# Performance work log

Measured on AMD Instinct MI355X. Metric: run time of the kernel, lower is better.

## Reference

```python
import jax, jax.numpy as jnp
import numpy as np

ALPHA = 0.5  # learn_alpha=False -> constant

def _init(key, shape, fan_in):
    return jax.random.normal(key, shape, dtype=jnp.float32) / np.sqrt(fan_in)

def setup_inputs() -> dict:
    key = jax.random.key(0)
    ks = jax.random.split(key, 12)
    B, S, N, F, H, E = 4, 8, 4000, 64, 128, 32000
    x_seq = jax.random.normal(ks[0], (B, S, N, F), dtype=jnp.float32)
    edge_index = jax.random.randint(ks[1], (B, S, 2, E), 0, N, dtype=jnp.int32)
    edge_weight = jax.random.uniform(ks[2], (B, S, E), dtype=jnp.float32)
    params = dict(
        W0_s=_init(ks[3], (H, F), F), b0_s=jnp.zeros((H,), jnp.float32),
        W0_d=_init(ks[4], (H, F), F), b0_d=jnp.zeros((H,), jnp.float32),
        W1_s=_init(ks[5], (H, H), H), b1_s=jnp.zeros((H,), jnp.float32),
        W1_d=_init(ks[6], (H, H), H), b1_d=jnp.zeros((H,), jnp.float32),
        lstm_Wih=_init(ks[7], (4 * H, H), H), lstm_Whh=_init(ks[8], (4 * H, H), H),
        lstm_bih=jnp.zeros((4 * H,), jnp.float32), lstm_bhh=jnp.zeros((4 * H,), jnp.float32),
        Wp=_init(ks[9], (F, H), H), bp=jnp.zeros((F,), jnp.float32),
    )
    return {"x_seq": x_seq, "edge_index": edge_index, "edge_weight": edge_weight, **params}

def _dir_gcn(x, src, dst, ew, Ws, bs, Wd, bd):
    # x: [N, Fin]. DirGCN: alpha * W_s(A_hat x) + (1-alpha) * W_d(A_hat^T x)
    # with symmetric directed normalization D_out^{-1/2} A D_in^{-1/2}.
    N = x.shape[0]
    deg_out = jax.ops.segment_sum(ew, src, num_segments=N)
    deg_in = jax.ops.segment_sum(ew, dst, num_segments=N)
    inv_out = jnp.where(deg_out > 0, jax.lax.rsqrt(jnp.maximum(deg_out, 1e-12)), 0.0)
    inv_in = jnp.where(deg_in > 0, jax.lax.rsqrt(jnp.maximum(deg_in, 1e-12)), 0.0)
    norm = ew * inv_out[src] * inv_in[dst]                         # [E]
    agg_f = jax.ops.segment_sum(norm[:, None] * x[src], dst, num_segments=N)  # A_hat x
    agg_b = jax.ops.segment_sum(norm[:, None] * x[dst], src, num_segments=N)  # A_hat^T x
    return ALPHA * (agg_f @ Ws.T + bs) + (1.0 - ALPHA) * (agg_b @ Wd.T + bd)

def reference(x_seq, edge_index, edge_weight, W0_s, b0_s, W0_d, b0_d,
              W1_s, b1_s, W1_d, b1_d, lstm_Wih, lstm_Whh, lstm_bih, lstm_bhh, Wp, bp):
    B, S, N, F = x_seq.shape
    H = W0_s.shape[0]
    G = B * S
    # fuse the per-(batch, timestep) python loops into one batched graph pass
    x = x_seq.reshape(G, N, F)
    src = edge_index[:, :, 0, :].reshape(G, -1)
    dst = edge_index[:, :, 1, :].reshape(G, -1)
    ew = edge_weight.reshape(G, -1)
    conv = jax.vmap(_dir_gcn, in_axes=(0, 0, 0, 0, None, None, None, None))
    h = conv(x, src, dst, ew, W0_s, b0_s, W0_d, b0_d)   # dropout is a no-op in eval mode
    h = conv(h, src, dst, ew, W1_s, b1_s, W1_d, b1_d)   # [G, N, H]
    # faithful to original: [B, S*N, H].reshape(B*N, S, H) (order-preserving flatten)
    seq = h.reshape(B * N, S, H)
    # single-layer unidirectional LSTM, batch_first; pytorch gate order i,f,g,o
    def step(carry, x_t):
        hprev, c = carry
        gates = x_t @ lstm_Wih.T + lstm_bih + hprev @ lstm_Whh.T + lstm_bhh
        i, f, g, o = jnp.split(gates, 4, axis=-1)
        c = jax.nn.sigmoid(f) * c + jax.nn.sigmoid(i) * jnp.tanh(g)
        hn = jax.nn.sigmoid(o) * jnp.tanh(c)
        return (hn, c), None
    h0 = jnp.zeros((B * N, H), x_seq.dtype)
    (h_last, _), _ = jax.lax.scan(step, (h0, h0), seq.transpose(1, 0, 2))
    return h_last.reshape(B, N, H) @ Wp.T + bp           # [B, N, num_features]
```

## Files before the change

### kernel.cpp

```cpp
#include <hip/hip_runtime.h>
#include <hip/hip_bf16.h>

#define B_  4
#define S_  8
#define N_  4000
#define F_  64
#define H_  128
#define E_  32000
#define G_  (B_*S_)
#define GN_ (G_*N_)
#define M_  (B_*N_)
#define GE_ (G_*E_)
#define HALF_GN 64000
#define HALF_M  8000
#define NBLK_   8
#define EPB_    (E_/NBLK_)

#define OFF_W0S 0
#define OFF_B0S 8192
#define OFF_W0D 8320
#define OFF_B0D 16512
#define OFF_W1S 16640
#define OFF_B1S 33024
#define OFF_W1D 33152
#define OFF_B1D 49536
#define OFF_WIH 49664
#define OFF_WHH 115200
#define OFF_BIH 180736
#define OFF_BHH 181248
#define OFF_WP  181760
#define OFF_BP  189952
#define WCV_TOTAL 190016

#define WS_FLAG   0
#define WS_WCV    16
#define WS_WPH    190032
#define WS_WPC    222800
#define WS_BIASC  288336
#define WS_DEGO   288848
#define WS_DEGI   416848
#define WS_CNTI   544848
#define WS_CNTO   672848
#define WS_RPI    800848
#define WS_RPO    928880
#define WS_CSRI   1312912
#define WS_CSRO   3360912
#define WS_X2     5408912
#define WS_PART   9608912
#define WS_HB     21792912
#define WS_GT     29984912
#define WS_WC0    46368912

typedef __attribute__((ext_vector_type(8))) short bf16x8;
typedef __attribute__((ext_vector_type(4))) float f32x4;
typedef __attribute__((ext_vector_type(8))) unsigned short ushort8;

__device__ inline float bfu2f(unsigned short u){ union{unsigned int i; float f;} v; v.i=((unsigned int)u)<<16; return v.f; }
__device__ inline unsigned short f2bfu(float f){ __hip_bfloat16 b = __float2bfloat16(f); return *(unsigned short*)&b; }
__device__ inline float rcpf(float x){ return __builtin_amdgcn_rcpf(x); }
__device__ inline float sigmf(float x){ return rcpf(1.0f + __expf(-x)); }
__device__ inline float tanhfast(float x){ return 1.0f - 2.0f*rcpf(1.0f + __expf(2.0f*x)); }
__device__ inline float loadf(const void* p, long i, int isf32){
    return isf32 ? ((const float*)p)[i]
                 : __bfloat162float(((const __hip_bfloat16*)p)[i]);
}
__device__ inline float4 cvtbf4(ushort4 u){
    float4 f;
    f.x = __uint_as_float(((unsigned)u.x)<<16);
    f.y = __uint_as_float(((unsigned)u.y)<<16);
    f.z = __uint_as_float(((unsigned)u.z)<<16);
    f.w = __uint_as_float(((unsigned)u.w)<<16);
    return f;
}

__global__ void sniff_kernel(const unsigned int* __restrict__ ew, int* __restrict__ flag){
    __shared__ int s;
    if (threadIdx.x == 0) s = 0;
    __syncthreads();
    unsigned int lo = ew[threadIdx.x] & 0xFFFFu;
    if (lo > 0x3F80u) atomicOr(&s, 1);
    __syncthreads();
    if (threadIdx.x == 0) flag[0] = s;
}

struct WSeg { const void* src; int base; int n; };
struct WDesc { WSeg seg[14]; };
__global__ void convert_weights(WDesc d, float* __restrict__ dst, const int* __restrict__ flag){
    int isf32 = flag[0];
    int idx = blockIdx.x*256 + threadIdx.x;
    #pragma unroll
    for (int s=0;s<14;s++){
        int off = idx - d.seg[s].base;
        if (off >= 0 && off < d.seg[s].n){
            dst[idx] = loadf(d.seg[s].src, off, isf32);
            return;
        }
    }
}

__global__ void repack_whh(const float* __restrict__ wcv, unsigned short* __restrict__ whb){
    int idx = blockIdx.x*256 + threadIdx.x;
    whb[idx] = f2bfu(wcv[OFF_WHH + idx]);
}

__global__ void repack_wc0(const float* __restrict__ wcv, unsigned short* __restrict__ wc0){
    int idx = blockIdx.x*256 + threadIdx.x;
    int k = idx & 127, n = idx >> 7;
    float v = (k < 64) ? 0.5f*wcv[OFF_W0S + n*64 + k] : 0.5f*wcv[OFF_W0D + n*64 + (k-64)];
    wc0[idx] = f2bfu(v);
}

__global__ void xcvt_kernel(const void* __restrict__ x, const int* __restrict__ flag,
                            unsigned short* __restrict__ Xb){
    long idx = (long)blockIdx.x*256 + threadIdx.x;
    if (idx >= (long)GN_*64) return;
    Xb[idx] = f2bfu(loadf(x, idx, flag[0]));
}

__global__ __launch_bounds__(256) void compose_wc(const float* __restrict__ wcv,
                                                  unsigned short* __restrict__ wpc){
    int n = blockIdx.x;
    int k = threadIdx.x;
    const float* wih = wcv + OFF_WIH + n*128;
    const float* w1  = (k < 128) ? (wcv + OFF_W1S + k) : (wcv + OFF_W1D + (k-128));
    float s = 0.f;
    for (int h=0; h<128; h++) s += wih[h] * w1[h*128];
    wpc[n*256 + k] = f2bfu(0.5f * s);
}

__global__ void compose_bias(const float* __restrict__ wcv, float* __restrict__ biasc){
    int n = blockIdx.x*256 + threadIdx.x;
    if (n >= 512) return;
    float s = wcv[OFF_BIH+n] + wcv[OFF_BHH+n];
    const float* wih = wcv + OFF_WIH + n*128;
    for (int h=0; h<128; h++) s += wih[h] * 0.5f*(wcv[OFF_B1S+h] + wcv[OFF_B1D+h]);
    biasc[n] = s;
}

__global__ __launch_bounds__(1024) void hist_kernel(
        const int* __restrict__ ei, const void* __restrict__ ew, const int* __restrict__ flag,
        float* __restrict__ part){
    __shared__ float wdo[N_], wdi[N_];
    __shared__ int   co[N_],  ci[N_];
    int xcd  = blockIdx.x & 7;
    int r2   = blockIdx.x >> 3;
    int g    = xcd*4 + (r2 & 3);
    int b    = r2 >> 2;
    int tid  = threadIdx.x;
    int isf32 = flag[0];
    for (int i=tid;i<N_;i+=1024){ wdo[i]=0.f; wdi[i]=0.f; co[i]=0; ci[i]=0; }
    __syncthreads();
    const int* eib = ei + g*2*E_;
    int e0 = b*EPB_;
    for (int e=e0+tid; e<e0+EPB_; e+=1024){
        int s = eib[e], d = eib[E_+e];
        float w = loadf(ew, (long)g*E_+e, isf32);
        atomicAdd(&wdo[s], w); atomicAdd(&wdi[d], w);
        atomicAdd(&co[s], 1);  atomicAdd(&ci[d], 1);
    }
    __syncthreads();
    float* Pdo = part + (size_t)(0*G_ + g)*NBLK_*N_ + (size_t)b*N_;
    float* Pdi = part + (size_t)(1*G_ + g)*NBLK_*N_ + (size_t)b*N_;
    int*   Pci = (int*)part + (size_t)(2*G_ + g)*NBLK_*N_ + (size_t)b*N_;
    int*   Pco = (int*)part + (size_t)(3*G_ + g)*NBLK_*N_ + (size_t)b*N_;
    for (int i=tid;i<N_;i+=1024){
        Pdo[i] = wdo[i]; Pdi[i] = wdi[i];
        Pci[i] = ci[i];  Pco[i] = co[i];
    }
}

__global__ __launch_bounds__(256) void reduce_hist(
        float* __restrict__ part,
        float* __restrict__ deg_o, float* __restrict__ deg_i,
        int* __restrict__ cnt_in, int* __restrict__ cnt_out){
    int g = blockIdx.x >> 4;
    int n = (blockIdx.x & 15)*256 + threadIdx.x;
    if (n >= N_) return;
    float* Pdo = part + (size_t)(0*G_ + g)*NBLK_*N_;
    float* Pdi = part + (size_t)(1*G_ + g)*NBLK_*N_;
    int*   Pci = (int*)part + (size_t)(2*G_ + g)*NBLK_*N_;
    int*   Pco = (int*)part + (size_t)(3*G_ + g)*NBLK_*N_;
    float sdo = 0.f, sdi = 0.f;
    int sci = 0, sco = 0;
    #pragma unroll
    for (int b=0;b<NBLK_;b++){
        size_t idx = (size_t)b*N_ + n;
        sdo += Pdo[idx]; sdi += Pdi[idx];
        int vi = Pci[idx], vo = Pco[idx];
        Pci[idx] = sci;  Pco[idx] = sco;
        sci += vi; sco += vo;
    }
    deg_o[g*N_+n] = sdo; deg_i[g*N_+n] = sdi;
    cnt_in[g*N_+n] = sci; cnt_out[g*N_+n] = sco;
}

__global__ __launch_bounds__(256) void scan_kernel(
        const int* __restrict__ cnt_in, const int* __restrict__ cnt_out,
        int* __restrict__ rp_in, int* __restrict__ rp_out){
    __shared__ int part[256], pref[256];
    int g = blockIdx.x & 31, dir = blockIdx.x >> 5;
    const int* cnt = (dir ? cnt_out : cnt_in) + g*N_;
    int* rp  = (dir ? rp_out  : rp_in)  + g*(N_+1);
    int tid = threadIdx.x, base = tid*16;
    int sum = 0;
    for (int i=0;i<16;i++){ int p = base+i; if (p < N_) sum += cnt[p]; }
    part[tid] = sum;
    __syncthreads();
    if (tid == 0){ int run = 0; for (int j=0;j<256;j++){ pref[j] = run; run += part[j]; } }
    __syncthreads();
    int run = pref[tid];
    for (int i=0;i<16;i++){
        int p = base+i;
        if (p < N_){ rp[p] = run; run += cnt[p]; }
    }
    if (tid == 255) rp[N_] = run;
}

__global__ __launch_bounds__(1024) void fill_kernel(
        const int* __restrict__ ei, const void* __restrict__ ew,
        const int* __restrict__ flag,
        const float* __restrict__ deg_o, const float* __restrict__ deg_i,
        const int* __restrict__ rp_in, const int* __restrict__ rp_out,
        const float* __restrict__ part,
        int2* __restrict__ csr_in, int2* __restrict__ csr_out){
    __shared__ int lci[N_], lco[N_];
    int xcd  = blockIdx.x & 7;
    int r2   = blockIdx.x >> 3;
    int g    = xcd*4 + (r2 & 3);
    int b    = r2 >> 2;
    int tid  = threadIdx.x;
    int isf32 = flag[0];
    for (int i=tid;i<N_;i+=1024){ lci[i]=0; lco[i]=0; }
    __syncthreads();
    const int* eib = ei + g*2*E_;
    const int* cumI = (const int*)part + (size_t)(2*G_ + g)*NBLK_*N_ + (size_t)b*N_;
    const int* cumO = (const int*)part + (size_t)(3*G_ + g)*NBLK_*N_ + (size_t)b*N_;
    const int* rpi = rp_in  + g*(N_+1);
    const int* rpo = rp_out + g*(N_+1);
    int2* ci = csr_in  + (long)g*E_;
    int2* co = csr_out + (long)g*E_;
    int e0 = b*EPB_;
    for (int e=e0+tid; e<e0+EPB_; e+=1024){
        int s = eib[e], d = eib[E_+e];
        float dout = deg_o[g*N_+s], din = deg_i[g*N_+d];
        float io = dout > 0.f ? rsqrtf(fmaxf(dout, 1e-12f)) : 0.f;
        float ii = din  > 0.f ? rsqrtf(fmaxf(din , 1e-12f)) : 0.f;
        float nrm = loadf(ew, (long)g*E_ + e, isf32) * io * ii;
        int li = atomicAdd(&lci[d], 1);
        ci[rpi[d] + cumI[d] + li] = make_int2(s, __float_as_int(nrm));
        int lo = atomicAdd(&lco[s], 1);
        co[rpo[s] + cumO[s] + lo] = make_int2(d, __float_as_int(nrm));
    }
}

__global__ __launch_bounds__(256) void g0fused(
        const int* __restrict__ rp_in, const int* __restrict__ rp_out,
        const int2* __restrict__ csr_in, const int2* __restrict__ csr_out,
        const unsigned short* __restrict__ Xb, const unsigned short* __restrict__ wc0,
        const float* __restrict__ wcv, __hip_bfloat16* __restrict__ Hb){
    __shared__ unsigned short As[64*144];
    int xcd  = blockIdx.x & 7;
    int tile = blockIdx.x >> 3;
    int m0   = (xcd*250 + tile)*64;
    int tid  = threadIdx.x;

    int gid = tid >> 3, li = tid & 7;
    #pragma unroll
    for (int t=0; t<4; t++){
        int task = t*32 + gid;
        int dir  = task >> 6, r = task & 63;
        int grow = m0 + r;
        int g = grow / N_;  int n = grow - g*N_;
        const int*  rp  = (dir ? rp_out : rp_in) + g*(N_+1);
        const int2* csr = (dir ? csr_out : csr_in) + (long)g*E_;
        int pb = rp[n], pe = rp[n+1];
        int plast = max(pe - 1, 0);
        const unsigned short* base = Xb + (size_t)g*N_*64;
        float acc[8];
        #pragma unroll
        for (int j=0;j<8;j++) acc[j] = 0.f;
        for (int p=pb; p<pe; p+=4){
            float w4[4]; ushort8 v4[4];
            #pragma unroll
            for (int i=0;i<4;i++){
                int pi = p+i;
                int2 ent = csr[min(pi, plast)];
                w4[i] = (pi < pe) ? __int_as_float(ent.y) : 0.f;
                v4[i] = *(const ushort8*)(base + ent.x*64 + li*8);
            }
            #pragma unroll
            for (int i=0;i<4;i++)
                #pragma unroll
                for (int j=0;j<8;j++)
                    acc[j] += w4[i]*bfu2f(v4[i][j]);
        }
        ushort8 o;
        #pragma unroll
        for (int j=0;j<8;j++) o[j] = f2bfu(acc[j]);
        *(ushort8*)(&As[r*144 + dir*64 + li*8]) = o;
    }
    __syncthreads();

    int wave = tid >> 6, lane = tid & 63;
    int quad = lane >> 4, l16 = lane & 15;
    int colb = wave*16 + l16;
    bf16x8 bq[2][4];
    f32x4 acc[2][4];
    #pragma unroll
    for (int s=0;s<2;s++){
        #pragma unroll
        for (int ks=0;ks<4;ks++)
            bq[s][ks] = *(const bf16x8*)(wc0 + (size_t)(colb + s*64)*128 + ks*32 + quad*8);
        #pragma unroll
        for (int t=0;t<4;t++) acc[s][t] = (f32x4){0.f,0.f,0.f,0.f};
    }
    #pragma unroll
    for (int ks=0;ks<4;ks++){
        #pragma unroll
        for (int t=0;t<4;t++){
            bf16x8 a = *(const bf16x8*)(&As[(t*16 + l16)*144 + ks*32 + quad*8]);
            acc[0][t] = __builtin_amdgcn_mfma_f32_16x16x32_bf16(a, bq[0][ks], acc[0][t], 0, 0, 0);
            acc[1][t] = __builtin_amdgcn_mfma_f32_16x16x32_bf16(a, bq[1][ks], acc[1][t], 0, 0, 0);
        }
    }
    #pragma unroll
    for (int s=0;s<2;s++){
        int col = colb + s*64;
        float bias = 0.5f*(wcv[OFF_B0S+col] + wcv[OFF_B0D+col]);
        #pragma unroll
        for (int t=0;t<4;t++)
            #pragma unroll
            for (int r=0;r<4;r++)
                Hb[(size_t)(m0 + t*16 + quad*4 + r)*128 + col] = __float2bfloat16(acc[s][t][r] + bias);
    }
}

__global__ __launch_bounds__(512) void ggfused(
        const int* __restrict__ rp_in, const int* __restrict__ rp_out,
        const int2* __restrict__ csr_in, const int2* __restrict__ csr_out,
        const unsigned short* __restrict__ hb,
        const unsigned short* __restrict__ wpc, const float* __restrict__ biasc,
        unsigned short* __restrict__ gates, int gn_base){
    __shared__ unsigned short As[64*272];
    int xcd  = blockIdx.x & 7;
    int tile = blockIdx.x >> 3;
    int m0   = (xcd*125 + tile)*64;
    int tid  = threadIdx.x;

    int gid = tid >> 4, li = tid & 15;
    #pragma unroll
    for (int t=0; t<4; t++){
        int task = t*32 + gid;
        int dir  = task >> 6, r = task & 63;
        int grow = gn_base + m0 + r;
        int g = grow / N_;  int n = grow - g*N_;
        const int*  rp  = (dir ? rp_out : rp_in) + g*(N_+1);
        const int2* csr = (dir ? csr_out : csr_in) + (long)g*E_;
        int pb = rp[n], pe = rp[n+1];
        int plast = max(pe - 1, 0);
        const unsigned short* base = hb + (size_t)g*N_*128;
        float acc[8];
        #pragma unroll
        for (int j=0;j<8;j++) acc[j] = 0.f;
        for (int p=pb; p<pe; p+=4){
            float w4[4]; ushort8 v4[4];
            #pragma unroll
            for (int i=0;i<4;i++){
                int pi = p+i;
                int2 ent = csr[min(pi, plast)];
                w4[i] = (pi < pe) ? __int_as_float(ent.y) : 0.f;
                v4[i] = *(const ushort8*)(base + ent.x*128 + li*8);
            }
            #pragma unroll
            for (int i=0;i<4;i++)
                #pragma unroll
                for (int j=0;j<8;j++)
                    acc[j] += w4[i]*bfu2f(v4[i][j]);
        }
        ushort8 o;
        #pragma unroll
        for (int j=0;j<8;j++) o[j] = f2bfu(acc[j]);
        *(ushort8*)(&As[r*272 + dir*128 + li*8]) = o;
    }
    __syncthreads();

    int w = tid >> 6, lane = tid & 63;
    int quad = lane >> 4, l16 = lane & 15;
    for (int cs=0; cs<4; cs++){
        int col = cs*128 + w*16 + l16;
        bf16x8 bq[8];
        #pragma unroll
        for (int ks=0;ks<8;ks++)
            bq[ks] = *(const bf16x8*)(wpc + (size_t)col*256 + ks*32 + quad*8);
        f32x4 acc[4];
        #pragma unroll
        for (int t=0;t<4;t++) acc[t] = (f32x4){0.f,0.f,0.f,0.f};
        #pragma unroll
        for (int ks=0;ks<8;ks++)
            #pragma unroll
            for (int t=0;t<4;t++){
                bf16x8 a = *(const bf16x8*)(&As[(t*16 + l16)*272 + ks*32 + quad*8]);
                acc[t] = __builtin_amdgcn_mfma_f32_16x16x32_bf16(a, bq[ks], acc[t], 0, 0, 0);
            }
        float bc = biasc[col];
        #pragma unroll
        for (int t=0;t<4;t++)
            #pragma unroll
            for (int r=0;r<4;r++){
                int grow = m0 + t*16 + quad*4 + r;
                gates[(size_t)(grow>>3)*4096 + (size_t)col*8 + (grow&7)] = f2bfu(acc[t][r] + bc);
            }
    }
}

__global__ __launch_bounds__(512) void lstm7(
        const unsigned short* __restrict__ gates3, int mbase,
        const unsigned short* __restrict__ whb,
        const float* __restrict__ wcv, const int* __restrict__ flag,
        void* __restrict__ out){
    __shared__ unsigned short hsh[16*128];
    int tid  = threadIdx.x;
    int w    = tid >> 6;
    int lane = tid & 63;
    int quad = lane >> 4, l15 = lane & 15;
    int mlb  = blockIdx.x * 16;
    int m0   = mbase + mlb;
    int isf32 = flag[0];

    ushort8 pg[4][4];
    const unsigned short* gb = gates3 + (size_t)mlb*4096 + (size_t)(w*16 + l15)*8;
    #pragma unroll
    for (int g=0; g<4; g++)
        #pragma unroll
        for (int r=0; r<4; r++)
            pg[g][r] = *(const ushort8*)(gb + (size_t)(quad*4+r)*4096 + (size_t)g*1024);

    bf16x8 bfrag[4][4];
    #pragma unroll
    for (int g=0; g<4; g++)
        #pragma unroll
        for (int kt=0; kt<4; kt++)
            bfrag[g][kt] = *(const bf16x8*)(whb + (size_t)(g*128 + w*16 + l15)*128 + kt*32 + quad*8);

    for (int t=tid; t<16*128; t+=512) hsh[t] = 0;
    f32x4 c = (f32x4){0.f,0.f,0.f,0.f};
    __syncthreads();

    #pragma unroll
    for (int step=0; step<8; step++){
        f32x4 acc[4];
        #pragma unroll
        for (int g=0; g<4; g++)
            #pragma unroll
            for (int r=0; r<4; r++)
                acc[g][r] = bfu2f(pg[g][r][step]);
        #pragma unroll
        for (int kt=0; kt<4; kt++){
            bf16x8 a = *(const bf16x8*)(&hsh[l15*128 + (((kt*4+quad) ^ (l15&15))<<3)]);
            #pragma unroll
            for (int g=0; g<4; g++)
                acc[g] = __builtin_amdgcn_mfma_f32_16x16x32_bf16(a, bfrag[g][kt], acc[g], 0, 0, 0);
        }
        float hnew[4];
        #pragma unroll
        for (int r=0; r<4; r++){
            float gi = sigmf(acc[0][r]), gf = sigmf(acc[1][r]);
            float gg = tanhfast(acc[2][r]), go = sigmf(acc[3][r]);
            float cc = gf*c[r] + gi*gg;
            c[r] = cc;
            hnew[r] = go*tanhfast(cc);
        }
        __syncthreads();
        #pragma unroll
        for (int r=0; r<4; r++){
            int row = quad*4 + r;
            int idx = w*16 + l15;
            hsh[row*128 + (((idx>>3) ^ (row&15))<<3) + (idx&7)] = f2bfu(hnew[r]);
        }
        __syncthreads();
    }
    int r  = tid >> 5;
    int q0 = (tid & 31) * 2;
    float p0 = wcv[OFF_BP + q0], p1 = wcv[OFF_BP + q0 + 1];
    for (int k4=0;k4<32;k4++){
        float4 hv = cvtbf4(*(const ushort4*)(&hsh[r*128 + (((k4>>1) ^ (r&15))<<3) + (k4&1)*4]));
        float4 w0 = *(const float4*)(wcv + OFF_WP + q0*128 + k4*4);
        float4 w1 = *(const float4*)(wcv + OFF_WP + (q0+1)*128 + k4*4);
        p0 += w0.x*hv.x + w0.y*hv.y + w0.z*hv.z + w0.w*hv.w;
        p1 += w1.x*hv.x + w1.y*hv.y + w1.z*hv.z + w1.w*hv.w;
    }
    long o = (long)(m0+r)*64 + q0;
    if (isf32){ ((float*)out)[o] = p0; ((float*)out)[o+1] = p1; }
    else { ((__hip_bfloat16*)out)[o] = __float2bfloat16(p0);
           ((__hip_bfloat16*)out)[o+1] = __float2bfloat16(p1); }
}

extern "C" void kernel_launch(void* const* d_in, const int* in_sizes, int n_in,
                              void* d_out, int out_size, void* d_ws, size_t ws_size,
                              hipStream_t stream){
    const void* x_seq      = d_in[0];
    const int*  edge_index = (const int*)d_in[1];
    const void* edge_weight= d_in[2];

    float* ws    = (float*)d_ws;
    int*   flag  = (int*)(ws + WS_FLAG);
    float* wcv   = ws + WS_WCV;
    unsigned short* whb = (unsigned short*)(ws + WS_WPH);
    unsigned short* wpc = (unsigned short*)(ws + WS_WPC);
    unsigned short* wc0 = (unsigned short*)(ws + WS_WC0);
    float* biasc = ws + WS_BIASC;
    float* deg_o = ws + WS_DEGO;
    float* deg_i = ws + WS_DEGI;
    int*   cnt_i = (int*)(ws + WS_CNTI);
    int*   cnt_o = (int*)(ws + WS_CNTO);
    int*   rp_i  = (int*)(ws + WS_RPI);
    int*   rp_o  = (int*)(ws + WS_RPO);
    float* partb = ws + WS_PART;
    int2*  csr_i = (int2*)(ws + WS_CSRI);
    int2*  csr_o = (int2*)(ws + WS_CSRO);
    unsigned short* Xb = (unsigned short*)(ws + WS_X2);
    __hip_bfloat16* Hb = (__hip_bfloat16*)(ws + WS_HB);
    unsigned short* GT = (unsigned short*)(ws + WS_GT);

    sniff_kernel<<<1, 256, 0, stream>>>((const unsigned int*)edge_weight, flag);
    WDesc wd;
    wd.seg[0]  = { d_in[3],  OFF_W0S, 8192  };
    wd.seg[1]  = { d_in[4],  OFF_B0S, 128   };
    wd.seg[2]  = { d_in[5],  OFF_W0D, 8192  };
    wd.seg[3]  = { d_in[6],  OFF_B0D, 128   };
    wd.seg[4]  = { d_in[7],  OFF_W1S, 16384 };
    wd.seg[5]  = { d_in[8],  OFF_B1S, 128   };
    wd.seg[6]  = { d_in[9],  OFF_W1D, 16384 };
    wd.seg[7]  = { d_in[10], OFF_B1D, 128   };
    wd.seg[8]  = { d_in[11], OFF_WIH, 65536 };
    wd.seg[9]  = { d_in[12], OFF_WHH, 65536 };
    wd.seg[10] = { d_in[13], OFF_BIH, 512   };
    wd.seg[11] = { d_in[14], OFF_BHH, 512   };
    wd.seg[12] = { d_in[15], OFF_WP,  8192  };
    wd.seg[13] = { d_in[16], OFF_BP,  64    };
    convert_weights<<<(WCV_TOTAL+255)/256, 256, 0, stream>>>(wd, wcv, flag);
    repack_whh<<<256, 256, 0, stream>>>(wcv, whb);
    repack_wc0<<<64, 256, 0, stream>>>(wcv, wc0);
    compose_wc<<<512, 256, 0, stream>>>(wcv, wpc);
    compose_bias<<<2, 256, 0, stream>>>(wcv, biasc);
    xcvt_kernel<<<(GN_*64+255)/256, 256, 0, stream>>>(x_seq, flag, Xb);

    hist_kernel<<<G_*NBLK_, 1024, 0, stream>>>(edge_index, edge_weight, flag, partb);
    reduce_hist<<<G_*16, 256, 0, stream>>>(partb, deg_o, deg_i, cnt_i, cnt_o);
    scan_kernel<<<64, 256, 0, stream>>>(cnt_i, cnt_o, rp_i, rp_o);
    fill_kernel<<<G_*NBLK_, 1024, 0, stream>>>(edge_index, edge_weight, flag,
                                               deg_o, deg_i, rp_i, rp_o, partb, csr_i, csr_o);

    g0fused<<<GN_/64, 256, 0, stream>>>(rp_i, rp_o, csr_i, csr_o, Xb, wc0, wcv, Hb);

    ggfused<<<HALF_GN/64, 512, 0, stream>>>(rp_i, rp_o, csr_i, csr_o,
                                            (const unsigned short*)Hb, wpc, biasc, GT, 0);
    lstm7<<<HALF_M/16, 512, 0, stream>>>(GT, 0, whb, wcv, flag, d_out);

    ggfused<<<HALF_GN/64, 512, 0, stream>>>(rp_i, rp_o, csr_i, csr_o,
                                            (const unsigned short*)Hb, wpc, biasc, GT, HALF_GN);
    lstm7<<<HALF_M/16, 512, 0, stream>>>(GT, HALF_M, whb, wcv, flag, d_out);
}
```

Baseline: 515.9 us.

## Fuse second GCN layer and LSTM into one kernel via shared-memory gates

Merges the second graph-conv kernel, which wrote LSTM input gates to global memory, with the LSTM kernel. Each 64-row tile keeps its gates in LDS and runs the 8-step LSTM for its 8 sequences directly. This removes the gate round trip through global memory and two launches per half. In exchange, half of each 16-row MFMA tile is padding (only 8 sequences per block), and LDS use per block rises, which may lower occupancy.

New measurement: 593.5 us. 1.15x slower.

```diff
diff --git a/kernel.cpp b/kernel.cpp
--- a/kernel.cpp
+++ b/kernel.cpp
@@ -11,8 +11,6 @@
 #define GN_ (G_*N_)
 #define M_  (B_*N_)
 #define GE_ (G_*E_)
-#define HALF_GN 64000
-#define HALF_M  8000
 #define NBLK_   8
 #define EPB_    (E_/NBLK_)
 
@@ -335,24 +333,30 @@
     }
 }
 
-__global__ __launch_bounds__(512) void ggfused(
+__global__ __launch_bounds__(512) void gglstm(
         const int* __restrict__ rp_in, const int* __restrict__ rp_out,
         const int2* __restrict__ csr_in, const int2* __restrict__ csr_out,
         const unsigned short* __restrict__ hb,
         const unsigned short* __restrict__ wpc, const float* __restrict__ biasc,
-        unsigned short* __restrict__ gates, int gn_base){
+        const unsigned short* __restrict__ whb, const float* __restrict__ wcv,
+        const int* __restrict__ flag, void* __restrict__ out){
     __shared__ unsigned short As[64*272];
+    __shared__ unsigned short gsh[64*520];
+    __shared__ unsigned short hsh[16*128];
     int xcd  = blockIdx.x & 7;
     int tile = blockIdx.x >> 3;
-    int m0   = (xcd*125 + tile)*64;
+    int m0   = (xcd*250 + tile)*64;
     int tid  = threadIdx.x;
+    int isf32 = flag[0];
+
+    for (int t=tid; t<16*128; t+=512) hsh[t] = 0;
 
     int gid = tid >> 4, li = tid & 15;
     #pragma unroll
     for (int t=0; t<4; t++){
         int task = t*32 + gid;
         int dir  = task >> 6, r = task & 63;
-        int grow = gn_base + m0 + r;
+        int grow = m0 + r;
         int g = grow / N_;  int n = grow - g*N_;
         const int*  rp  = (dir ? rp_out : rp_in) + g*(N_+1);
         const int2* csr = (dir ? csr_out : csr_in) + (long)g*E_;
@@ -407,34 +411,13 @@
         for (int t=0;t<4;t++)
             #pragma unroll
             for (int r=0;r<4;r++){
-                int grow = m0 + t*16 + quad*4 + r;
-                gates[(size_t)(grow>>3)*4096 + (size_t)col*8 + (grow&7)] = f2bfu(acc[t][r] + bc);
+                int r8 = t*16 + quad*4 + r;
+                gsh[r8*520 + col] = f2bfu(acc[t][r] + bc);
             }
     }
-}
-
-__global__ __launch_bounds__(512) void lstm7(
-        const unsigned short* __restrict__ gates3, int mbase,
-        const unsigned short* __restrict__ whb,
-        const float* __restrict__ wcv, const int* __restrict__ flag,
-        void* __restrict__ out){
-    __shared__ unsigned short hsh[16*128];
-    int tid  = threadIdx.x;
-    int w    = tid >> 6;
-    int lane = tid & 63;
-    int quad = lane >> 4, l15 = lane & 15;
-    int mlb  = blockIdx.x * 16;
-    int m0   = mbase + mlb;
-    int isf32 = flag[0];
-
-    ushort8 pg[4][4];
-    const unsigned short* gb = gates3 + (size_t)mlb*4096 + (size_t)(w*16 + l15)*8;
-    #pragma unroll
-    for (int g=0; g<4; g++)
-        #pragma unroll
-        for (int r=0; r<4; r++)
-            pg[g][r] = *(const ushort8*)(gb + (size_t)(quad*4+r)*4096 + (size_t)g*1024);
-
+    __syncthreads();
+
+    int l15 = lane & 15;
     bf16x8 bfrag[4][4];
     #pragma unroll
     for (int g=0; g<4; g++)
@@ -442,21 +425,21 @@
         for (int kt=0; kt<4; kt++)
             bfrag[g][kt] = *(const bf16x8*)(whb + (size_t)(g*128 + w*16 + l15)*128 + kt*32 + quad*8);
 
-    for (int t=tid; t<16*128; t+=512) hsh[t] = 0;
     f32x4 c = (f32x4){0.f,0.f,0.f,0.f};
-    __syncthreads();
-
     #pragma unroll
     for (int step=0; step<8; step++){
         f32x4 acc[4];
         #pragma unroll
         for (int g=0; g<4; g++)
             #pragma unroll
-            for (int r=0; r<4; r++)
-                acc[g][r] = bfu2f(pg[g][r][step]);
+            for (int r=0; r<4; r++){
+                int row = quad*4 + r;
+                acc[g][r] = (row < 8)
+                    ? bfu2f(gsh[(8*row + step)*520 + g*128 + w*16 + l15]) : 0.f;
+            }
         #pragma unroll
         for (int kt=0; kt<4; kt++){
-            bf16x8 a = *(const bf16x8*)(&hsh[l15*128 + (((kt*4+quad) ^ (l15&15))<<3)]);
+            bf16x8 a = *(const bf16x8*)(&hsh[l15*128 + (((kt*4+quad) ^ l15)<<3)]);
             #pragma unroll
             for (int g=0; g<4; g++)
                 acc[g] = __builtin_amdgcn_mfma_f32_16x16x32_bf16(a, bfrag[g][kt], acc[g], 0, 0, 0);
@@ -474,25 +457,25 @@
         #pragma unroll
         for (int r=0; r<4; r++){
             int row = quad*4 + r;
-            int idx = w*16 + l15;
-            hsh[row*128 + (((idx>>3) ^ (row&15))<<3) + (idx&7)] = f2bfu(hnew[r]);
+            if (row < 8){
+                int idx = w*16 + l15;
+                hsh[row*128 + (((idx>>3) ^ row)<<3) + (idx&7)] = f2bfu(hnew[r]);
+            }
         }
         __syncthreads();
     }
-    int r  = tid >> 5;
-    int q0 = (tid & 31) * 2;
-    float p0 = wcv[OFF_BP + q0], p1 = wcv[OFF_BP + q0 + 1];
+
+    int r = tid >> 6;
+    int q = tid & 63;
+    float p = wcv[OFF_BP + q];
     for (int k4=0;k4<32;k4++){
-        float4 hv = cvtbf4(*(const ushort4*)(&hsh[r*128 + (((k4>>1) ^ (r&15))<<3) + (k4&1)*4]));
-        float4 w0 = *(const float4*)(wcv + OFF_WP + q0*128 + k4*4);
-        float4 w1 = *(const float4*)(wcv + OFF_WP + (q0+1)*128 + k4*4);
-        p0 += w0.x*hv.x + w0.y*hv.y + w0.z*hv.z + w0.w*hv.w;
-        p1 += w1.x*hv.x + w1.y*hv.y + w1.z*hv.z + w1.w*hv.w;
-    }
-    long o = (long)(m0+r)*64 + q0;
-    if (isf32){ ((float*)out)[o] = p0; ((float*)out)[o+1] = p1; }
-    else { ((__hip_bfloat16*)out)[o] = __float2bfloat16(p0);
-           ((__hip_bfloat16*)out)[o+1] = __float2bfloat16(p1); }
+        float4 hv = cvtbf4(*(const ushort4*)(&hsh[r*128 + (((k4>>1) ^ r)<<3) + (k4&1)*4]));
+        float4 w0 = *(const float4*)(wcv + OFF_WP + q*128 + k4*4);
+        p += w0.x*hv.x + w0.y*hv.y + w0.z*hv.z + w0.w*hv.w;
+    }
+    long o = (long)((m0>>3) + r)*64 + q;
+    if (isf32) ((float*)out)[o] = p;
+    else       ((__hip_bfloat16*)out)[o] = __float2bfloat16(p);
 }
 
 extern "C" void kernel_launch(void* const* d_in, const int* in_sizes, int n_in,
@@ -520,7 +503,6 @@
     int2*  csr_o = (int2*)(ws + WS_CSRO);
     unsigned short* Xb = (unsigned short*)(ws + WS_X2);
     __hip_bfloat16* Hb = (__hip_bfloat16*)(ws + WS_HB);
-    unsigned short* GT = (unsigned short*)(ws + WS_GT);
 
     sniff_kernel<<<1, 256, 0, stream>>>((const unsigned int*)edge_weight, flag);
     WDesc wd;
@@ -553,11 +535,7 @@
 
     g0fused<<<GN_/64, 256, 0, stream>>>(rp_i, rp_o, csr_i, csr_o, Xb, wc0, wcv, Hb);
 
-    ggfused<<<HALF_GN/64, 512, 0, stream>>>(rp_i, rp_o, csr_i, csr_o,
-                                            (const unsigned short*)Hb, wpc, biasc, GT, 0);
-    lstm7<<<HALF_M/16, 512, 0, stream>>>(GT, 0, whb, wcv, flag, d_out);
-
-    ggfused<<<HALF_GN/64, 512, 0, stream>>>(rp_i, rp_o, csr_i, csr_o,
-                                            (const unsigned short*)Hb, wpc, biasc, GT, HALF_GN);
-    lstm7<<<HALF_M/16, 512, 0, stream>>>(GT, HALF_M, whb, wcv, flag, d_out);
-}
+    gglstm<<<GN_/64, 512, 0, stream>>>(rp_i, rp_o, csr_i, csr_o,
+                                       (const unsigned short*)Hb, wpc, biasc,
+                                       whb, wcv, flag, d_out);
+}
```
